# Optimization experiments

Hardware: AMD Instinct MI355X
Metric: run time of the kernel (lower is better)

The kernel has to match this reference:

```python
import jax, jax.numpy as jnp
import numpy as np

D_MODEL = 1024
D_K = 1024
D_V = 1024

def setup_inputs() -> dict:
    key = jax.random.key(0)
    k1, k2, k3, k4 = jax.random.split(key, 4)
    X = jax.random.normal(k1, (4, 2048, D_MODEL), dtype=jnp.float32)
    # nn.Linear weights have shape (out_features, in_features)
    s = 1.0 / np.sqrt(D_MODEL)
    W_q = jax.random.uniform(k2, (D_K, D_MODEL), dtype=jnp.float32, minval=-s, maxval=s)
    W_k = jax.random.uniform(k3, (D_K, D_MODEL), dtype=jnp.float32, minval=-s, maxval=s)
    W_v = jax.random.uniform(k4, (D_V, D_MODEL), dtype=jnp.float32, minval=-s, maxval=s)
    return {"X": X, "W_q": W_q, "W_k": W_k, "W_v": W_v}

def reference(X, W_q, W_k, W_v):
    # Q,K,V: [b, m, d]
    Q = jnp.einsum('bmd,kd->bmk', X, W_q)
    K = jnp.einsum('bmd,kd->bmk', X, W_k)
    V = jnp.einsum('bmd,vd->bmv', X, W_v)
    scale = 1.0 / jnp.sqrt(jnp.asarray(D_K, dtype=jnp.float32))
    A = jnp.einsum('bmk,bnk->bmn', Q, K) * scale  # [b, m, m]
    weights = jax.nn.softmax(A, axis=-1)
    context = jnp.einsum('bmn,bnv->bmv', weights, V)
    return (context, weights)
```

## Files before the change

kernel.cpp:

```cpp
#include <hip/hip_runtime.h>
#include <math.h>


typedef __bf16 bf16;
typedef __bf16 bf16x4 __attribute__((ext_vector_type(4)));
typedef __bf16 bf16x8 __attribute__((ext_vector_type(8)));
typedef float  f32x4  __attribute__((ext_vector_type(4)));

#define GLD_TO_LDS(g, l) __builtin_amdgcn_global_load_lds(                    \
    (const __attribute__((address_space(1))) void*)(g),                       \
    (__attribute__((address_space(3))) void*)(l), 16, 0, 0)

#define STAGE_A(tc, P, h) do {                                                \
    const bf16* _s = aRow + (long)((h) * 128) * lda + (long)(tc) * 64;        \
    char* _d = ldsA + (P) * 32768 + (h) * 16384 + t * 16;                     \
    GLD_TO_LDS(_s, _d); GLD_TO_LDS(_s + 64L * lda, _d + 8192); } while (0)
#define STAGE_B(tc, P, h) do {                                                \
    const bf16* _s = bRow + (long)((h) * 128) * ldb + (long)(tc) * 64;        \
    char* _d = ldsB + (P) * 32768 + (h) * 16384 + t * 16;                     \
    GLD_TO_LDS(_s, _d); GLD_TO_LDS(_s + 64L * ldb, _d + 8192); } while (0)
#define VMCNT4 asm volatile("s_waitcnt vmcnt(4)" ::: "memory")

template<int OUT, bool SPLITK>
__global__ __launch_bounds__(512, 2)
void gemm8(const bf16* __restrict__ A, const bf16* __restrict__ B,
           void* __restrict__ Cp, int nkt, int lda, int ldb, int ldc,
           long sA, long sB, long sC, long sKa, long sKb, float alpha)
{
    __shared__ __align__(16) char smem[131072];
    char* ldsA = smem;
    char* ldsB = smem + 65536;

    const int bz = SPLITK ? (blockIdx.z >> 1) : blockIdx.z;
    A += bz * sA;
    B += bz * sB;
    if (SPLITK) {
        const int ck = blockIdx.z & 1;
        A += ck * sKa;
        B += ck * sKb;
    }

    const int t    = threadIdx.x;
    const int wid  = t >> 6;
    const int lane = t & 63;
    const int wr   = wid >> 2;
    const int wn   = wid & 3;
    const int fr   = lane & 15;
    const int g    = lane >> 4;
    const int brow = blockIdx.y * 256;
    const int bcol = blockIdx.x * 256;

    const int  srow = t >> 3;
    const int  scol = ((t & 7) ^ ((t >> 3) & 7)) * 8;
    const bf16* aRow = A + (long)(brow + srow) * lda + scol;
    const bf16* bRow = B + (long)(bcol + srow) * ldb + scol;

    const int  c0  = (g * 16) ^ ((fr & 7) << 4);
    const int  c1  = c0 ^ 64;
    const char* aRd = ldsA + (wr * 128 + fr) * 128;
    const char* bRd = ldsB + (wn * 64 + fr) * 128;

    f32x4 acc[8][4] = {};
    bf16x8 bfrag[4][2];

    STAGE_A(0, 0, 0); STAGE_A(0, 0, 1); STAGE_B(0, 0, 0); STAGE_B(0, 0, 1);
    STAGE_A(1, 1, 0); STAGE_A(1, 1, 1); STAGE_B(1, 1, 0); STAGE_B(1, 1, 1);
    asm volatile("s_waitcnt vmcnt(8)" ::: "memory");
    __builtin_amdgcn_s_barrier();

    const int niter = nkt >> 1;
    for (int it = 0; it < niter; ++it) {
        const int cur = 2 * it;
        const int tc2 = (cur + 2 < nkt) ? cur + 2 : nkt - 1;
        const int tc3 = (cur + 3 < nkt) ? cur + 3 : nkt - 1;
        #pragma unroll
        for (int ph = 0; ph < 8; ++ph) {
            const int q = ph & 3;
            const int P = ph >> 2;

            if (q == 0) {
                #pragma unroll
                for (int n = 0; n < 4; ++n) {
                    bfrag[n][0] = *reinterpret_cast<const bf16x8*>(
                        bRd + P * 32768 + n * 2048 + c0);
                    bfrag[n][1] = *reinterpret_cast<const bf16x8*>(
                        bRd + P * 32768 + n * 2048 + c1);
                }
            }
            bf16x8 af[2][2];
            #pragma unroll
            for (int i = 0; i < 2; ++i) {
                af[i][0] = *reinterpret_cast<const bf16x8*>(
                    aRd + P * 32768 + (2 * q + i) * 2048 + c0);
                af[i][1] = *reinterpret_cast<const bf16x8*>(
                    aRd + P * 32768 + (2 * q + i) * 2048 + c1);
            }

            if (ph == 0) STAGE_A(cur + 1, 1, 0);
            if (ph == 1) STAGE_A(cur + 1, 1, 1);
            if (ph == 2) STAGE_B(tc2, 0, 0);
            if (ph == 3) { STAGE_B(tc2, 0, 1); VMCNT4; }
            if (ph == 4) STAGE_A(tc2, 0, 0);
            if (ph == 5) STAGE_A(tc2, 0, 1);
            if (ph == 6) STAGE_B(tc3, 1, 0);
            if (ph == 7) { STAGE_B(tc3, 1, 1); VMCNT4; }

            __builtin_amdgcn_s_barrier();
            __builtin_amdgcn_s_setprio(1);
            #pragma unroll
            for (int i = 0; i < 2; ++i)
                #pragma unroll
                for (int n = 0; n < 4; ++n) {
                    acc[2 * q + i][n] = __builtin_amdgcn_mfma_f32_16x16x32_bf16(
                        af[i][0], bfrag[n][0], acc[2 * q + i][n], 0, 0, 0);
                    acc[2 * q + i][n] = __builtin_amdgcn_mfma_f32_16x16x32_bf16(
                        af[i][1], bfrag[n][1], acc[2 * q + i][n], 0, 0, 0);
                }
            __builtin_amdgcn_s_setprio(0);
            __builtin_amdgcn_s_barrier();
        }
    }

    #pragma unroll
    for (int m = 0; m < 8; ++m) {
        #pragma unroll
        for (int n = 0; n < 4; ++n) {
            const int ccol = bcol + wn * 64 + n * 16 + fr;
            #pragma unroll
            for (int rr = 0; rr < 4; ++rr) {
                const long crow = brow + wr * 128 + m * 16 + g * 4 + rr;
                const float v = acc[m][n][rr] * alpha;
                if constexpr (OUT == 0) {
                    ((float*)Cp + bz * sC)[crow * ldc + ccol] = v;
                } else if constexpr (OUT == 1) {
                    ((bf16*)Cp + bz * sC)[crow * ldc + ccol] = (bf16)v;
                } else {
                    atomicAdd(&((float*)Cp + bz * sC)[crow * ldc + ccol], v);
                }
            }
        }
    }
}

__global__ __launch_bounds__(256)
void cast_bf16(const float* __restrict__ in, bf16* __restrict__ out, int n4)
{
    int i = blockIdx.x * 256 + threadIdx.x;
    const int stride = gridDim.x * 256;
    for (; i < n4; i += stride) {
        float4 v = reinterpret_cast<const float4*>(in)[i];
        bf16x4 o = { (bf16)v.x, (bf16)v.y, (bf16)v.z, (bf16)v.w };
        reinterpret_cast<bf16x4*>(out)[i] = o;
    }
}

__global__ __launch_bounds__(256)
void cast_w3(const float* __restrict__ Wq, const float* __restrict__ Wk,
             const float* __restrict__ Wv, bf16* __restrict__ dst)
{
    const int idx = blockIdx.x * 256 + threadIdx.x;
    const float* src;
    int off;
    if (idx < 262144)      { src = Wq; off = idx; }
    else if (idx < 524288) { src = Wk; off = idx - 262144; }
    else                   { src = Wv; off = idx - 524288; }
    float4 v = reinterpret_cast<const float4*>(src)[off];
    bf16x4 o = { (bf16)v.x, (bf16)v.y, (bf16)v.z, (bf16)v.w };
    reinterpret_cast<bf16x4*>(dst)[idx] = o;
}

__global__ __launch_bounds__(256)
void zerofill(float4* __restrict__ p, int n4)
{
    const int i = blockIdx.x * 256 + threadIdx.x;
    if (i < n4) p[i] = float4{0.f, 0.f, 0.f, 0.f};
}

__global__ __launch_bounds__(256)
void softmax_rows(float* __restrict__ W, bf16* __restrict__ Wb)
{
    float* p  = W  + (long)blockIdx.x * 2048;
    bf16*  pb = Wb + (long)blockIdx.x * 2048;
    const int tid  = threadIdx.x;
    const int wid  = tid >> 6;
    const int lane = tid & 63;

    float4 v0 = reinterpret_cast<const float4*>(p)[tid];
    float4 v1 = reinterpret_cast<const float4*>(p)[tid + 256];

    float m = fmaxf(fmaxf(fmaxf(v0.x, v0.y), fmaxf(v0.z, v0.w)),
                    fmaxf(fmaxf(v1.x, v1.y), fmaxf(v1.z, v1.w)));
    #pragma unroll
    for (int off = 32; off >= 1; off >>= 1)
        m = fmaxf(m, __shfl_xor(m, off));

    __shared__ float red[8];
    if (lane == 0) red[wid] = m;
    __syncthreads();
    m = fmaxf(fmaxf(red[0], red[1]), fmaxf(red[2], red[3]));

    v0.x = __expf(v0.x - m); v0.y = __expf(v0.y - m);
    v0.z = __expf(v0.z - m); v0.w = __expf(v0.w - m);
    v1.x = __expf(v1.x - m); v1.y = __expf(v1.y - m);
    v1.z = __expf(v1.z - m); v1.w = __expf(v1.w - m);

    float s = (v0.x + v0.y + v0.z + v0.w) + (v1.x + v1.y + v1.z + v1.w);
    #pragma unroll
    for (int off = 32; off >= 1; off >>= 1)
        s += __shfl_xor(s, off);
    __syncthreads();
    if (lane == 0) red[4 + wid] = s;
    __syncthreads();
    s = (red[4] + red[5]) + (red[6] + red[7]);

    const float inv = 1.f / s;
    v0.x *= inv; v0.y *= inv; v0.z *= inv; v0.w *= inv;
    v1.x *= inv; v1.y *= inv; v1.z *= inv; v1.w *= inv;
    reinterpret_cast<float4*>(p)[tid]       = v0;
    reinterpret_cast<float4*>(p)[tid + 256] = v1;
    bf16x4 b0 = { (bf16)v0.x, (bf16)v0.y, (bf16)v0.z, (bf16)v0.w };
    bf16x4 b1 = { (bf16)v1.x, (bf16)v1.y, (bf16)v1.z, (bf16)v1.w };
    reinterpret_cast<bf16x4*>(pb)[tid]       = b0;
    reinterpret_cast<bf16x4*>(pb)[tid + 256] = b1;
}

extern "C" void kernel_launch(void* const* d_in, const int* in_sizes, int n_in,
                              void* d_out, int out_size, void* d_ws, size_t ws_size,
                              hipStream_t stream)
{
    const float* X  = (const float*)d_in[0];
    const float* Wq = (const float*)d_in[1];
    const float* Wk = (const float*)d_in[2];
    const float* Wv = (const float*)d_in[3];

    const long BT = 4L * 2048;
    const long D  = 1024;
    const long S  = 2048;
    const long MiB = 1024 * 1024;

    float* ctx = (float*)d_out;
    float* wts = (float*)d_out + BT * D;

    char* ws   = (char*)d_ws;
    bf16* Xb   = (bf16*)(ws);
    bf16* Wqkb = (bf16*)(ws + 16 * MiB);
    bf16* Wvb  = (bf16*)(ws + 20 * MiB);
    bf16* QKb  = (bf16*)(ws + 22 * MiB);
    bf16* Vtb  = (bf16*)(ws + 54 * MiB);
    bf16* Wbf  = (bf16*)(ws);

    dim3 blk(256), blk8(512);

    cast_bf16<<<dim3(2048), blk, 0, stream>>>(X, Xb, (int)(BT * D / 4));
    cast_w3<<<dim3(3072), blk, 0, stream>>>(Wq, Wk, Wv, Wqkb);
    zerofill<<<dim3(8192), blk, 0, stream>>>((float4*)ctx, (int)(BT * D / 4));

    gemm8<1, false><<<dim3(8, 32, 1), blk8, 0, stream>>>(
        Xb, Wqkb, QKb, 16, 1024, 1024, 2048, 0, 0, 0, 0, 0, 1.f);
    gemm8<1, false><<<dim3(32, 4, 1), blk8, 0, stream>>>(
        Wvb, Xb, Vtb, 16, 1024, 1024, 8192, 0, 0, 0, 0, 0, 1.f);
    gemm8<0, false><<<dim3(8, 8, 4), blk8, 0, stream>>>(
        QKb, QKb + 1024, wts, 16, 2048, 2048, 2048,
        S * 2048, S * 2048, S * S, 0, 0, 0.03125f);
    softmax_rows<<<dim3(BT), blk, 0, stream>>>(wts, Wbf);

    gemm8<2, true><<<dim3(4, 8, 8), blk8, 0, stream>>>(
        Wbf, Vtb, ctx, 16, 2048, 8192, 1024,
        S * S, S, S * D, 1024, 1024, 1.f);
}
```

Measured before the change: 344.5 us.

## Add 256x128 tile variant and drop split-K atomics for context GEMM

Templates the GEMM kernel on the N tile width (256 or 128), which shrinks the B LDS buffer, the accumulator count and the staging waits for the narrow variant. The V projection and the final weights×V GEMM now use 256x128 tiles. This doubles their block count in place of the 2-way split-K with atomicAdd. That removes the zero-fill kernel and the atomic float adds into the context output, at the cost of each context block running the full K of 2048 serially (32 k-tiles) and fewer MFMAs per loaded A fragment.

Measured after the change: 290.6 us. -15.6%, faster.

```diff
diff --git a/kernel.cpp b/kernel.cpp
--- a/kernel.cpp
+++ b/kernel.cpp
@@ -16,29 +16,29 @@
     char* _d = ldsA + (P) * 32768 + (h) * 16384 + t * 16;                     \
     GLD_TO_LDS(_s, _d); GLD_TO_LDS(_s + 64L * lda, _d + 8192); } while (0)
 #define STAGE_B(tc, P, h) do {                                                \
-    const bf16* _s = bRow + (long)((h) * 128) * ldb + (long)(tc) * 64;        \
-    char* _d = ldsB + (P) * 32768 + (h) * 16384 + t * 16;                     \
-    GLD_TO_LDS(_s, _d); GLD_TO_LDS(_s + 64L * ldb, _d + 8192); } while (0)
-#define VMCNT4 asm volatile("s_waitcnt vmcnt(4)" ::: "memory")
-
-template<int OUT, bool SPLITK>
+    const bf16* _s = bRow + (long)((h) * (BN / 2)) * ldb + (long)(tc) * 64;   \
+    char* _d = ldsB + (P) * (BN * 128) + (h) * (BN * 64) + t * 16;            \
+    GLD_TO_LDS(_s, _d);                                                       \
+    if constexpr (BN == 256) GLD_TO_LDS(_s + 64L * ldb, _d + 8192); } while (0)
+#define VMCNT_S do {                                                          \
+    if constexpr (BN == 256) asm volatile("s_waitcnt vmcnt(4)" ::: "memory"); \
+    else                     asm volatile("s_waitcnt vmcnt(2)" ::: "memory"); \
+    } while (0)
+
+template<int OUT, int BN>
 __global__ __launch_bounds__(512, 2)
 void gemm8(const bf16* __restrict__ A, const bf16* __restrict__ B,
            void* __restrict__ Cp, int nkt, int lda, int ldb, int ldc,
-           long sA, long sB, long sC, long sKa, long sKb, float alpha)
-{
-    __shared__ __align__(16) char smem[131072];
+           long sA, long sB, long sC, float alpha)
+{
+    constexpr int NB = BN / 64;
+    __shared__ __align__(16) char smem[65536 + BN * 256];
     char* ldsA = smem;
     char* ldsB = smem + 65536;
 
-    const int bz = SPLITK ? (blockIdx.z >> 1) : blockIdx.z;
+    const int bz = blockIdx.z;
     A += bz * sA;
     B += bz * sB;
-    if (SPLITK) {
-        const int ck = blockIdx.z & 1;
-        A += ck * sKa;
-        B += ck * sKb;
-    }
 
     const int t    = threadIdx.x;
     const int wid  = t >> 6;
@@ -48,7 +48,7 @@
     const int fr   = lane & 15;
     const int g    = lane >> 4;
     const int brow = blockIdx.y * 256;
-    const int bcol = blockIdx.x * 256;
+    const int bcol = blockIdx.x * BN;
 
     const int  srow = t >> 3;
     const int  scol = ((t & 7) ^ ((t >> 3) & 7)) * 8;
@@ -58,14 +58,15 @@
     const int  c0  = (g * 16) ^ ((fr & 7) << 4);
     const int  c1  = c0 ^ 64;
     const char* aRd = ldsA + (wr * 128 + fr) * 128;
-    const char* bRd = ldsB + (wn * 64 + fr) * 128;
-
-    f32x4 acc[8][4] = {};
-    bf16x8 bfrag[4][2];
+    const char* bRd = ldsB + (wn * (BN / 4) + fr) * 128;
+
+    f32x4 acc[8][NB] = {};
+    bf16x8 bfrag[NB][2];
 
     STAGE_A(0, 0, 0); STAGE_A(0, 0, 1); STAGE_B(0, 0, 0); STAGE_B(0, 0, 1);
     STAGE_A(1, 1, 0); STAGE_A(1, 1, 1); STAGE_B(1, 1, 0); STAGE_B(1, 1, 1);
-    asm volatile("s_waitcnt vmcnt(8)" ::: "memory");
+    if constexpr (BN == 256) asm volatile("s_waitcnt vmcnt(8)" ::: "memory");
+    else                     asm volatile("s_waitcnt vmcnt(6)" ::: "memory");
     __builtin_amdgcn_s_barrier();
 
     const int niter = nkt >> 1;
@@ -80,11 +81,11 @@
 
             if (q == 0) {
                 #pragma unroll
-                for (int n = 0; n < 4; ++n) {
+                for (int n = 0; n < NB; ++n) {
                     bfrag[n][0] = *reinterpret_cast<const bf16x8*>(
-                        bRd + P * 32768 + n * 2048 + c0);
+                        bRd + P * (BN * 128) + n * 2048 + c0);
                     bfrag[n][1] = *reinterpret_cast<const bf16x8*>(
-                        bRd + P * 32768 + n * 2048 + c1);
+                        bRd + P * (BN * 128) + n * 2048 + c1);
                 }
             }
             bf16x8 af[2][2];
@@ -99,18 +100,18 @@
             if (ph == 0) STAGE_A(cur + 1, 1, 0);
             if (ph == 1) STAGE_A(cur + 1, 1, 1);
             if (ph == 2) STAGE_B(tc2, 0, 0);
-            if (ph == 3) { STAGE_B(tc2, 0, 1); VMCNT4; }
+            if (ph == 3) { STAGE_B(tc2, 0, 1); VMCNT_S; }
             if (ph == 4) STAGE_A(tc2, 0, 0);
             if (ph == 5) STAGE_A(tc2, 0, 1);
             if (ph == 6) STAGE_B(tc3, 1, 0);
-            if (ph == 7) { STAGE_B(tc3, 1, 1); VMCNT4; }
+            if (ph == 7) { STAGE_B(tc3, 1, 1); VMCNT_S; }
 
             __builtin_amdgcn_s_barrier();
             __builtin_amdgcn_s_setprio(1);
             #pragma unroll
             for (int i = 0; i < 2; ++i)
                 #pragma unroll
-                for (int n = 0; n < 4; ++n) {
+                for (int n = 0; n < NB; ++n) {
                     acc[2 * q + i][n] = __builtin_amdgcn_mfma_f32_16x16x32_bf16(
                         af[i][0], bfrag[n][0], acc[2 * q + i][n], 0, 0, 0);
                     acc[2 * q + i][n] = __builtin_amdgcn_mfma_f32_16x16x32_bf16(
@@ -124,18 +125,16 @@
     #pragma unroll
     for (int m = 0; m < 8; ++m) {
         #pragma unroll
-        for (int n = 0; n < 4; ++n) {
-            const int ccol = bcol + wn * 64 + n * 16 + fr;
+        for (int n = 0; n < NB; ++n) {
+            const int ccol = bcol + wn * (BN / 4) + n * 16 + fr;
             #pragma unroll
             for (int rr = 0; rr < 4; ++rr) {
                 const long crow = brow + wr * 128 + m * 16 + g * 4 + rr;
                 const float v = acc[m][n][rr] * alpha;
                 if constexpr (OUT == 0) {
                     ((float*)Cp + bz * sC)[crow * ldc + ccol] = v;
-                } else if constexpr (OUT == 1) {
+                } else {
                     ((bf16*)Cp + bz * sC)[crow * ldc + ccol] = (bf16)v;
-                } else {
-                    atomicAdd(&((float*)Cp + bz * sC)[crow * ldc + ccol], v);
                 }
             }
         }
@@ -170,13 +169,6 @@
 }
 
 __global__ __launch_bounds__(256)
-void zerofill(float4* __restrict__ p, int n4)
-{
-    const int i = blockIdx.x * 256 + threadIdx.x;
-    if (i < n4) p[i] = float4{0.f, 0.f, 0.f, 0.f};
-}
-
-__global__ __launch_bounds__(256)
 void softmax_rows(float* __restrict__ W, bf16* __restrict__ Wb)
 {
     float* p  = W  + (long)blockIdx.x * 2048;
@@ -253,18 +245,17 @@
 
     cast_bf16<<<dim3(2048), blk, 0, stream>>>(X, Xb, (int)(BT * D / 4));
     cast_w3<<<dim3(3072), blk, 0, stream>>>(Wq, Wk, Wv, Wqkb);
-    zerofill<<<dim3(8192), blk, 0, stream>>>((float4*)ctx, (int)(BT * D / 4));
-
-    gemm8<1, false><<<dim3(8, 32, 1), blk8, 0, stream>>>(
-        Xb, Wqkb, QKb, 16, 1024, 1024, 2048, 0, 0, 0, 0, 0, 1.f);
-    gemm8<1, false><<<dim3(32, 4, 1), blk8, 0, stream>>>(
-        Wvb, Xb, Vtb, 16, 1024, 1024, 8192, 0, 0, 0, 0, 0, 1.f);
-    gemm8<0, false><<<dim3(8, 8, 4), blk8, 0, stream>>>(
+
+    gemm8<1, 256><<<dim3(8, 32, 1), blk8, 0, stream>>>(
+        Xb, Wqkb, QKb, 16, 1024, 1024, 2048, 0, 0, 0, 1.f);
+    gemm8<1, 128><<<dim3(64, 4, 1), blk8, 0, stream>>>(
+        Wvb, Xb, Vtb, 16, 1024, 1024, 8192, 0, 0, 0, 1.f);
+    gemm8<0, 256><<<dim3(8, 8, 4), blk8, 0, stream>>>(
         QKb, QKb + 1024, wts, 16, 2048, 2048, 2048,
-        S * 2048, S * 2048, S * S, 0, 0, 0.03125f);
+        S * 2048, S * 2048, S * S, 0.03125f);
     softmax_rows<<<dim3(BT), blk, 0, stream>>>(wts, Wbf);
 
-    gemm8<2, true><<<dim3(4, 8, 8), blk8, 0, stream>>>(
-        Wbf, Vtb, ctx, 16, 2048, 8192, 1024,
-        S * S, S, S * D, 1024, 1024, 1.f);
-}
+    gemm8<0, 128><<<dim3(8, 8, 4), blk8, 0, stream>>>(
+        Wbf, Vtb, ctx, 32, 2048, 8192, 1024,
+        S * S, S, S * D, 1.f);
+}
```
